# Performance work log

Hardware: AMD Instinct MI355X
Metric: run time of the kernel (lower is better)

## Reference

```python
import jax, jax.numpy as jnp
import numpy as np

NP_, NS_ = 100000, 10000      # num pdrugs / seffect nodes
FPD, FSE = 512, 768           # raw feature dims
H = 64                        # hidden_channels
E = 1_600_000                 # message-passing edges
L = 1_000_000                 # labeled edges (pos+neg)


def setup_inputs() -> dict:
    key = jax.random.key(0)
    ks = jax.random.split(key, 40)
    f32 = jnp.float32

    def nrm(k, shape, scale=0.05):
        return jax.random.normal(k, shape, f32) * scale

    inp = {}
    inp['x_pdrugs'] = jax.random.normal(ks[0], (NP_, FPD), f32)
    inp['x_seffect'] = jax.random.normal(ks[1], (NS_, FSE), f32)
    inp['node_id_pd'] = jnp.arange(NP_)
    inp['node_id_se'] = jnp.arange(NS_)
    inp['edge_index'] = jnp.stack([
        jax.random.randint(ks[2], (E,), 0, NP_),
        jax.random.randint(ks[3], (E,), 0, NS_)])
    # positive labeled edges + negative-sampled edges (label 0)
    inp['edge_label_index'] = jnp.stack([
        jax.random.randint(ks[4], (L,), 0, NP_),
        jax.random.randint(ks[5], (L,), 0, NS_)])
    inp['edge_label'] = jnp.concatenate(
        [jnp.ones(L // 2, f32), jnp.zeros(L - L // 2, f32)])

    # input projections + node embeddings
    inp['W_pd'] = nrm(ks[6], (FPD, H)); inp['b_pd'] = jnp.zeros((H,), f32)
    inp['W_se'] = nrm(ks[7], (FSE, H)); inp['b_se'] = jnp.zeros((H,), f32)
    inp['emb_pd'] = nrm(ks[8], (NP_, H), 1.0)
    inp['emb_se'] = nrm(ks[9], (NS_, H), 1.0)

    # hetero SAGEConv params: 2 layers x 2 edge types (p2s, s2p)
    i = 10
    for lyr in (1, 2):
        for et in ('p2s', 's2p'):
            inp[f'c{lyr}_{et}_Wl'] = nrm(ks[i], (H, H)); i += 1
            inp[f'c{lyr}_{et}_bl'] = jnp.zeros((H,), f32)
            inp[f'c{lyr}_{et}_Wr'] = nrm(ks[i], (H, H)); i += 1
    return inp


def _sage(x_src, x_dst, src_idx, dst_idx, n_dst, Wl, bl, Wr):
    # SAGEConv: lin_l(mean_j x_src[j]) + lin_r(x_dst)
    msg = x_src[src_idx]                                   # [E, H] gather
    agg = jax.ops.segment_sum(msg, dst_idx, num_segments=n_dst)
    deg = jax.ops.segment_sum(jnp.ones((src_idx.shape[0],), x_src.dtype),
                              dst_idx, num_segments=n_dst)
    mean = agg / jnp.clip(deg, 1.0)[:, None]
    return mean @ Wl + bl + x_dst @ Wr


def reference(x_pdrugs, x_seffect, edge_label,
              W_pd, b_pd, W_se, b_se, emb_pd, emb_se,
              c1_p2s_Wl, c1_p2s_bl, c1_p2s_Wr,
              c1_s2p_Wl, c1_s2p_bl, c1_s2p_Wr,
              c2_p2s_Wl, c2_p2s_bl, c2_p2s_Wr,
              c2_s2p_Wl, c2_s2p_bl, c2_s2p_Wr,
              node_id_pd, node_id_se, edge_index, edge_label_index):
    src, dst = edge_index[0], edge_index[1]  # pdrugs -> seffect

    # embed + linear fusion
    h_pd = x_pdrugs @ W_pd + b_pd + emb_pd[node_id_pd]
    h_se = x_seffect @ W_se + b_se + emb_se[node_id_se]

    # hetero GNN layer 1 (relu)
    se1 = jax.nn.relu(_sage(h_pd, h_se, src, dst, NS_, c1_p2s_Wl, c1_p2s_bl, c1_p2s_Wr))
    pd1 = jax.nn.relu(_sage(h_se, h_pd, dst, src, NP_, c1_s2p_Wl, c1_s2p_bl, c1_s2p_Wr))

    # hetero GNN layer 2 (no activation)
    se2 = _sage(pd1, se1, src, dst, NS_, c2_p2s_Wl, c2_p2s_bl, c2_p2s_Wr)
    pd2 = _sage(se1, pd1, dst, src, NP_, c2_s2p_Wl, c2_s2p_bl, c2_s2p_Wr)

    # edge-wise gather-dot classifier
    pred = jnp.sum(pd2[edge_label_index[0]] * se2[edge_label_index[1]], axis=-1)
    return (pred, edge_label)
```

## Files before the change

### kernel.cpp

```cpp
#include <hip/hip_runtime.h>

namespace {

constexpr int NP = 100000;
constexpr int NS = 10000;
constexpr int EC = 1600000;
constexpr int LC = 1000000;

constexpr int SH_S = 6;
constexpr int SH_P = 9;
constexpr int NBS = (NS + 63) >> SH_S;
constexpr int NBP = (NP + 511) >> SH_P;
constexpr int CHUNK = 8192;
constexpr int NBLK = (EC + CHUNK - 1) / CHUNK;

typedef short i16x8 __attribute__((ext_vector_type(8)));
typedef float f32x4 __attribute__((ext_vector_type(4)));

__device__ inline ushort f2bf(float f) {
  unsigned u = __float_as_uint(f);
  u += 0x7FFFu + ((u >> 16) & 1u);
  return (ushort)(u >> 16);
}
__device__ inline float bflo(uint v) { return __uint_as_float(v << 16); }
__device__ inline float bfhi(uint v) { return __uint_as_float(v & 0xffff0000u); }


__global__ void __launch_bounds__(256) k_bcount(const int* __restrict__ src,
                                                const int* __restrict__ dst,
                                                int* __restrict__ bcntS,
                                                int* __restrict__ bcntP, int E) {
  __shared__ int hS[256];
  __shared__ int hP[256];
  const int t = threadIdx.x;
  hS[t] = 0;
  hP[t] = 0;
  __syncthreads();
  const int base = blockIdx.x * CHUNK;
  const int end = min(base + CHUNK, E);
  for (int e = base + t; e < end; e += 256) {
    atomicAdd(&hS[dst[e] >> SH_S], 1);
    atomicAdd(&hP[src[e] >> SH_P], 1);
  }
  __syncthreads();
  if (t < NBS && hS[t]) atomicAdd(&bcntS[t], hS[t]);
  if (t < NBP && hP[t]) atomicAdd(&bcntP[t], hP[t]);
}

__global__ void __launch_bounds__(256) k_bscan(const int* __restrict__ bcntS,
                                               const int* __restrict__ bcntP,
                                               int* __restrict__ gbaseS,
                                               int* __restrict__ gbaseP,
                                               int* __restrict__ gcurS,
                                               int* __restrict__ gcurP) {
  __shared__ int s[256];
  const int t = threadIdx.x;
  int v = (t < NBS) ? bcntS[t] : 0;
  s[t] = v;
  __syncthreads();
  for (int off = 1; off < 256; off <<= 1) {
    int u = (t >= off) ? s[t - off] : 0;
    __syncthreads();
    s[t] += u;
    __syncthreads();
  }
  if (t < NBS) {
    int ex = s[t] - v;
    gbaseS[t] = ex;
    gcurS[t] = ex;
  }
  __syncthreads();
  v = (t < NBP) ? bcntP[t] : 0;
  s[t] = v;
  __syncthreads();
  for (int off = 1; off < 256; off <<= 1) {
    int u = (t >= off) ? s[t - off] : 0;
    __syncthreads();
    s[t] += u;
    __syncthreads();
  }
  if (t < NBP) {
    int ex = s[t] - v;
    gbaseP[t] = ex;
    gcurP[t] = ex;
  }
}

__global__ void __launch_bounds__(256) k_bscatter(const int* __restrict__ src,
                                                  const int* __restrict__ dst,
                                                  int* __restrict__ gcurS,
                                                  int* __restrict__ gcurP,
                                                  int* __restrict__ tmpS,
                                                  int* __restrict__ tmpP, int E) {
  __shared__ int hS[256];
  __shared__ int hP[256];
  const int t = threadIdx.x;
  hS[t] = 0;
  hP[t] = 0;
  __syncthreads();
  const int base = blockIdx.x * CHUNK;
  const int end = min(base + CHUNK, E);
  for (int e = base + t; e < end; e += 256) {
    atomicAdd(&hS[dst[e] >> SH_S], 1);
    atomicAdd(&hP[src[e] >> SH_P], 1);
  }
  __syncthreads();
  int myBaseS = 0, myBaseP = 0;
  if (t < NBS) {
    int c = hS[t];
    myBaseS = c ? atomicAdd(&gcurS[t], c) : 0;
  }
  if (t < NBP) {
    int c = hP[t];
    myBaseP = c ? atomicAdd(&gcurP[t], c) : 0;
  }
  __syncthreads();
  if (t < NBS) hS[t] = myBaseS;
  if (t < NBP) hP[t] = myBaseP;
  __syncthreads();
  for (int e = base + t; e < end; e += 256) {
    const int d = dst[e];
    const int s = src[e];
    int p = atomicAdd(&hS[d >> SH_S], 1);
    tmpS[p] = ((d & 63) << 17) | s;
    int q = atomicAdd(&hP[s >> SH_P], 1);
    tmpP[q] = ((s & 511) << 14) | d;
  }
}

template <int NN, int LBITS>
__global__ void __launch_bounds__(256) k_bfinal(const int* __restrict__ tmp,
                                                const int* __restrict__ gbase,
                                                const int* __restrict__ bcnt,
                                                int shift, int Nnodes,
                                                int* __restrict__ rowptr,
                                                int* __restrict__ deg,
                                                int* __restrict__ col) {
  __shared__ int ldeg[NN];
  __shared__ int lscan[512];
  const int b = blockIdx.x;
  const int t = threadIdx.x;
  const int n0 = b << shift;
  const int base = gbase[b];
  const int cnt = bcnt[b];
  for (int i = t; i < NN; i += 256) ldeg[i] = 0;
  __syncthreads();
  for (int j = t; j < cnt; j += 256) atomicAdd(&ldeg[tmp[base + j] >> LBITS], 1);
  __syncthreads();
  for (int i = t; i < 512; i += 256) lscan[i] = (i < NN) ? ldeg[i] : 0;
  __syncthreads();
  for (int off = 1; off < 512; off <<= 1) {
    const int i0 = t, i1 = t + 256;
    const int v0 = (i0 >= off) ? lscan[i0 - off] : 0;
    const int v1 = (i1 >= off) ? lscan[i1 - off] : 0;
    __syncthreads();
    lscan[i0] += v0;
    lscan[i1] += v1;
    __syncthreads();
  }
  for (int i = t; i < NN; i += 256) {
    const int n = n0 + i;
    if (n < Nnodes) {
      const int dg = ldeg[i];
      rowptr[n] = base + lscan[i] - dg;
      deg[n] = dg;
    }
  }
  __syncthreads();
  for (int i = t; i < NN; i += 256) lscan[i] -= ldeg[i];
  __syncthreads();
  for (int j = t; j < cnt; j += 256) {
    const int v = tmp[base + j];
    const int p = atomicAdd(&lscan[v >> LBITS], 1);
    col[base + p] = v & ((1 << LBITS) - 1);
  }
}


struct WtJob {
  const float* src;
  ushort* dst;
  int K;
  int stride;
  int off;
};
struct WtJobs {
  WtJob j[10];
};

__global__ void __launch_bounds__(256) k_wt_all(WtJobs jobs) {
  int e = blockIdx.x * 256 + threadIdx.x;
#pragma unroll
  for (int i = 0; i < 10; i++) {
    const int K = jobs.j[i].K;
    const int sz = K * 64;
    if (e < sz) {
      const int n = e / K;
      const int k = e - n * K;
      jobs.j[i].dst[(size_t)n * jobs.j[i].stride + jobs.j[i].off + k] =
          f2bf(jobs.j[i].src[(size_t)k * 64 + n]);
      return;
    }
    e -= sz;
  }
}


struct GJob {
  const void* A0;
  const void* A1;
  int KA0, sA0, sA1, K;
  const ushort* Wt;
  const float* bias;
  const float* emb;
  const int* nid;
  void* out;
  int M;
  int nblk;
};

template <bool RELU, bool EMB, bool ABF16, bool OBF16>
__global__ void __launch_bounds__(256) k_mgemm2(GJob ja, GJob jb) {
  __shared__ ushort Xs[64 * 72];
  __shared__ ushort Ws[64 * 72];
  const bool sec = (int)blockIdx.x >= ja.nblk;
  const GJob j = sec ? jb : ja;
  const int bid = sec ? ((int)blockIdx.x - ja.nblk) : (int)blockIdx.x;
  const int t = threadIdx.x;
  const int row0 = bid * 64;
  const int lane = t & 63;
  const int w = t >> 6;
  const int m16 = lane & 15;
  const int q = lane >> 4;
  const int M = j.M;
  const int K = j.K;
  const int KA0 = j.KA0;

  f32x4 acc[4];
#pragma unroll
  for (int nt = 0; nt < 4; nt++) acc[nt] = {0.f, 0.f, 0.f, 0.f};

  const int ksteps = K >> 6;
  for (int ks = 0; ks < ksteps; ks++) {
    const int k0 = ks << 6;
    uint4 wv[2];
#pragma unroll
    for (int i = 0; i < 2; i++) {
      const int u = t + i * 256;
      const int n = u >> 3;
      const int kk8 = (u & 7) << 3;
      wv[i] = *reinterpret_cast<const uint4*>(j.Wt + (size_t)n * K + k0 + kk8);
    }
    if constexpr (ABF16) {
      uint4 xv[2];
#pragma unroll
      for (int i = 0; i < 2; i++) {
        const int u = t + i * 256;
        const int row = u >> 3;
        const int k8 = (u & 7) << 3;
        const int gr = min(row0 + row, M - 1);
        const int kk = k0 + k8;
        const ushort* sp = (kk < KA0)
                               ? ((const ushort*)j.A0 + (size_t)gr * j.sA0 + kk)
                               : ((const ushort*)j.A1 + (size_t)gr * j.sA1 + (kk - KA0));
        xv[i] = *reinterpret_cast<const uint4*>(sp);
      }
      __syncthreads();
#pragma unroll
      for (int i = 0; i < 2; i++) {
        const int u = t + i * 256;
        const int row = u >> 3;
        const int k8 = (u & 7) << 3;
        *reinterpret_cast<uint4*>(&Xs[row * 72 + k8]) = xv[i];
      }
    } else {
      float4 xv[4];
#pragma unroll
      for (int i = 0; i < 4; i++) {
        const int u = t + i * 256;
        const int row = u >> 4;
        const int k4 = (u & 15) << 2;
        const int gr = min(row0 + row, M - 1);
        const int kk = k0 + k4;
        const float* sp = (kk < KA0)
                              ? ((const float*)j.A0 + (size_t)gr * j.sA0 + kk)
                              : ((const float*)j.A1 + (size_t)gr * j.sA1 + (kk - KA0));
        xv[i] = *reinterpret_cast<const float4*>(sp);
      }
      __syncthreads();
#pragma unroll
      for (int i = 0; i < 4; i++) {
        const int u = t + i * 256;
        const int row = u >> 4;
        const int k4 = (u & 15) << 2;
        ushort4 o;
        o.x = f2bf(xv[i].x);
        o.y = f2bf(xv[i].y);
        o.z = f2bf(xv[i].z);
        o.w = f2bf(xv[i].w);
        *reinterpret_cast<ushort4*>(&Xs[row * 72 + k4]) = o;
      }
    }
#pragma unroll
    for (int i = 0; i < 2; i++) {
      const int u = t + i * 256;
      const int n = u >> 3;
      const int kk8 = (u & 7) << 3;
      *reinterpret_cast<uint4*>(&Ws[n * 72 + kk8]) = wv[i];
    }
    __syncthreads();

    const ushort* ap = &Xs[(w * 16 + m16) * 72 + q * 8];
    const i16x8 a0 = *reinterpret_cast<const i16x8*>(ap);
    const i16x8 a1 = *reinterpret_cast<const i16x8*>(ap + 32);
#pragma unroll
    for (int nt = 0; nt < 4; nt++) {
      const ushort* bp = &Ws[(nt * 16 + m16) * 72 + q * 8];
      const i16x8 b0 = *reinterpret_cast<const i16x8*>(bp);
      const i16x8 b1 = *reinterpret_cast<const i16x8*>(bp + 32);
      acc[nt] = __builtin_amdgcn_mfma_f32_16x16x32_bf16(a0, b0, acc[nt], 0, 0, 0);
      acc[nt] = __builtin_amdgcn_mfma_f32_16x16x32_bf16(a1, b1, acc[nt], 0, 0, 0);
    }
    __syncthreads();
  }

  int grow[4];
  int nrow[4];
#pragma unroll
  for (int r = 0; r < 4; r++) {
    grow[r] = row0 + w * 16 + q * 4 + r;
    nrow[r] = (EMB && grow[r] < M) ? j.nid[grow[r]] : 0;
  }
#pragma unroll
  for (int nt = 0; nt < 4; nt++) {
    const int colv = nt * 16 + m16;
    const float bv = j.bias[colv];
#pragma unroll
    for (int r = 0; r < 4; r++) {
      if (grow[r] < M) {
        float v = acc[nt][r] + bv;
        if (EMB) v += j.emb[(size_t)nrow[r] * 64 + colv];
        if (RELU) v = fmaxf(v, 0.f);
        if (OBF16)
          ((ushort*)j.out)[(size_t)grow[r] * 64 + colv] = f2bf(v);
        else
          ((float*)j.out)[(size_t)grow[r] * 64 + colv] = v;
      }
    }
  }
}


__global__ void __launch_bounds__(256) k_agg2(
    const ushort* __restrict__ hS,
    const ushort* __restrict__ hP,
    const int* __restrict__ rpS, const int* __restrict__ degS, const int* __restrict__ colS,
    const int* __restrict__ rpP, const int* __restrict__ degP, const int* __restrict__ colP,
    ushort* __restrict__ outS,
    ushort* __restrict__ outP
) {
  int g = blockIdx.x * 4 + (threadIdx.x >> 6);
  const uint* hu;
  const int* rp;
  const int* deg;
  const int* col;
  uint* out;
  int node;
  if (g < NS) {
    hu = (const uint*)hS; rp = rpS; deg = degS; col = colS; out = (uint*)outS;
    node = g;
  } else {
    node = g - NS;
    if (node >= NP) return;
    hu = (const uint*)hP; rp = rpP; deg = degP; col = colP; out = (uint*)outP;
  }
  const int lane = threadIdx.x & 63;
  const int c = lane & 31;
  const int half = lane >> 5;
  const int beg = rp[node];
  const int cnt = deg[node];
  float a0 = 0.f, a1 = 0.f;
  int jj = 0;
  for (; jj + 16 <= cnt; jj += 16) {
    int n[8];
#pragma unroll
    for (int u = 0; u < 8; u++) n[u] = col[beg + jj + 2 * u + half];
#pragma unroll
    for (int u = 0; u < 8; u++) {
      const uint v = hu[(size_t)n[u] * 32 + c];
      a0 += bflo(v);
      a1 += bfhi(v);
    }
  }
  for (; jj + 2 <= cnt; jj += 2) {
    const uint v = hu[(size_t)col[beg + jj + half] * 32 + c];
    a0 += bflo(v);
    a1 += bfhi(v);
  }
  if (jj < cnt && half == 0) {
    const uint v = hu[(size_t)col[beg + jj] * 32 + c];
    a0 += bflo(v);
    a1 += bfhi(v);
  }
  a0 += __shfl_xor(a0, 32);
  a1 += __shfl_xor(a1, 32);
  if (half == 0) {
    const float d = (cnt > 0) ? (float)cnt : 1.f;
    const uint o = (uint)f2bf(a0 / d) | ((uint)f2bf(a1 / d) << 16);
    out[(size_t)node * 32 + c] = o;
  }
}


__global__ void __launch_bounds__(256) k_classify(const float* __restrict__ pd2,
                                                  const float* __restrict__ se2,
                                                  const int* __restrict__ i0,
                                                  const int* __restrict__ i1,
                                                  const float* __restrict__ elabel,
                                                  float* __restrict__ outF, int L,
                                                  int nClsBlk) {
  if ((int)blockIdx.x >= nClsBlk) {
    const int i = ((int)blockIdx.x - nClsBlk) * 256 + threadIdx.x;
    if (i < L / 4)
      reinterpret_cast<float4*>(outF + L)[i] =
          reinterpret_cast<const float4*>(elabel)[i];
    return;
  }
  const int e = blockIdx.x * 16 + (threadIdx.x >> 4);
  if (e >= L) return;
  const int l16 = threadIdx.x & 15;
  const int a = i0[e];
  const int b = i1[e];
  const float4 va = *reinterpret_cast<const float4*>(&pd2[(size_t)a * 64 + l16 * 4]);
  const float4 vb = *reinterpret_cast<const float4*>(&se2[(size_t)b * 64 + l16 * 4]);
  float v = va.x * vb.x + va.y * vb.y + va.z * vb.z + va.w * vb.w;
  v += __shfl_xor(v, 1, 16);
  v += __shfl_xor(v, 2, 16);
  v += __shfl_xor(v, 4, 16);
  v += __shfl_xor(v, 8, 16);
  if (l16 == 0) outF[e] = v;
}

}

extern "C" void kernel_launch(void* const* d_in, const int* in_sizes, int n_in,
                              void* d_out, int out_size, void* d_ws, size_t ws_size,
                              hipStream_t stream) {
  (void)in_sizes; (void)n_in; (void)out_size; (void)ws_size;
  const float* x_pd = (const float*)d_in[0];
  const float* x_se = (const float*)d_in[1];
  const int* nid_pd = (const int*)d_in[2];
  const int* nid_se = (const int*)d_in[3];
  const int* eidx = (const int*)d_in[4];
  const int* elidx = (const int*)d_in[5];
  const float* elabel = (const float*)d_in[6];
  const float* W_pd = (const float*)d_in[7];
  const float* b_pd = (const float*)d_in[8];
  const float* W_se = (const float*)d_in[9];
  const float* b_se = (const float*)d_in[10];
  const float* emb_pd = (const float*)d_in[11];
  const float* emb_se = (const float*)d_in[12];
  const float* c1_p2s_Wl = (const float*)d_in[13];
  const float* c1_p2s_bl = (const float*)d_in[14];
  const float* c1_p2s_Wr = (const float*)d_in[15];
  const float* c1_s2p_Wl = (const float*)d_in[16];
  const float* c1_s2p_bl = (const float*)d_in[17];
  const float* c1_s2p_Wr = (const float*)d_in[18];
  const float* c2_p2s_Wl = (const float*)d_in[19];
  const float* c2_p2s_bl = (const float*)d_in[20];
  const float* c2_p2s_Wr = (const float*)d_in[21];
  const float* c2_s2p_Wl = (const float*)d_in[22];
  const float* c2_s2p_bl = (const float*)d_in[23];
  const float* c2_s2p_Wr = (const float*)d_in[24];

  const int* src = eidx;
  const int* dst = eidx + EC;
  const int* li0 = elidx;
  const int* li1 = elidx + LC;

  char* ws = (char*)d_ws;
  size_t o = 0;
  auto alloc = [&](size_t bytes) -> char* {
    char* p = ws + o;
    o = (o + bytes + 255) & ~(size_t)255;
    return p;
  };
  ushort* h_pd = (ushort*)alloc((size_t)NP * 64 * 2);
  ushort* h_se = (ushort*)alloc((size_t)NS * 64 * 2);
  ushort* pd1 = (ushort*)alloc((size_t)NP * 64 * 2);
  ushort* se1 = (ushort*)alloc((size_t)NS * 64 * 2);
  ushort* agg_pd = (ushort*)alloc((size_t)NP * 64 * 2);
  ushort* agg_se = (ushort*)alloc((size_t)NS * 64 * 2);
  float* pd2 = (float*)alloc((size_t)NP * 64 * 4);
  float* se2 = (float*)alloc((size_t)NS * 64 * 4);
  int* col_se = (int*)alloc((size_t)EC * 4);
  int* col_pd = (int*)alloc((size_t)EC * 4);
  int* deg_se = (int*)alloc((size_t)NS * 4);
  int* deg_pd = (int*)alloc((size_t)NP * 4);
  int* rp_se = (int*)alloc((size_t)NS * 4);
  int* rp_pd = (int*)alloc((size_t)NP * 4);
  int* bcntS = (int*)alloc(1024);
  int* bcntP = (int*)alloc(1024);
  int* gbaseS = (int*)alloc(1024);
  int* gbaseP = (int*)alloc(1024);
  int* gcurS = (int*)alloc(1024);
  int* gcurP = (int*)alloc(1024);
  ushort* wt_pd = (ushort*)alloc((size_t)64 * 512 * 2);
  ushort* wt_se = (ushort*)alloc((size_t)64 * 768 * 2);
  ushort* wt_c1p2s = (ushort*)alloc((size_t)64 * 128 * 2);
  ushort* wt_c1s2p = (ushort*)alloc((size_t)64 * 128 * 2);
  ushort* wt_c2p2s = (ushort*)alloc((size_t)64 * 128 * 2);
  ushort* wt_c2s2p = (ushort*)alloc((size_t)64 * 128 * 2);

  int* tmpS = (int*)pd2;
  int* tmpP = tmpS + EC;

  hipMemsetAsync(bcntS, 0, 1024, stream);
  hipMemsetAsync(bcntP, 0, 1024, stream);

  k_bcount<<<NBLK, 256, 0, stream>>>(src, dst, bcntS, bcntP, EC);
  k_bscan<<<1, 256, 0, stream>>>(bcntS, bcntP, gbaseS, gbaseP, gcurS, gcurP);
  k_bscatter<<<NBLK, 256, 0, stream>>>(src, dst, gcurS, gcurP, tmpS, tmpP, EC);
  k_bfinal<64, 17><<<NBS, 256, 0, stream>>>(tmpS, gbaseS, bcntS, SH_S, NS, rp_se,
                                            deg_se, col_se);
  k_bfinal<512, 14><<<NBP, 256, 0, stream>>>(tmpP, gbaseP, bcntP, SH_P, NP, rp_pd,
                                             deg_pd, col_pd);

  {
    WtJobs jobs;
    jobs.j[0] = {W_pd, wt_pd, 512, 512, 0};
    jobs.j[1] = {W_se, wt_se, 768, 768, 0};
    jobs.j[2] = {c1_p2s_Wl, wt_c1p2s, 64, 128, 0};
    jobs.j[3] = {c1_p2s_Wr, wt_c1p2s, 64, 128, 64};
    jobs.j[4] = {c1_s2p_Wl, wt_c1s2p, 64, 128, 0};
    jobs.j[5] = {c1_s2p_Wr, wt_c1s2p, 64, 128, 64};
    jobs.j[6] = {c2_p2s_Wl, wt_c2p2s, 64, 128, 0};
    jobs.j[7] = {c2_p2s_Wr, wt_c2p2s, 64, 128, 64};
    jobs.j[8] = {c2_s2p_Wl, wt_c2s2p, 64, 128, 0};
    jobs.j[9] = {c2_s2p_Wr, wt_c2s2p, 64, 128, 64};
    const int tot = 64 * (512 + 768 + 8 * 64);
    k_wt_all<<<(tot + 255) / 256, 256, 0, stream>>>(jobs);
  }

  const int gP = (NP + 63) / 64;
  const int gS = (NS + 63) / 64;
  const int gAgg = (NS + NP) / 4;

  {
    GJob jp = {x_pd, nullptr, 512, 512, 0, 512, wt_pd, b_pd, emb_pd, nid_pd, h_pd, NP, gP};
    GJob js = {x_se, nullptr, 768, 768, 0, 768, wt_se, b_se, emb_se, nid_se, h_se, NS, gS};
    k_mgemm2<false, true, false, true><<<gP + gS, 256, 0, stream>>>(jp, js);
  }

  k_agg2<<<gAgg, 256, 0, stream>>>(h_pd, h_se, rp_se, deg_se, col_se, rp_pd, deg_pd,
                                   col_pd, agg_se, agg_pd);
  {
    GJob jp = {agg_pd, h_pd, 64, 64, 64, 128, wt_c1s2p, c1_s2p_bl, nullptr, nullptr, pd1, NP, gP};
    GJob js = {agg_se, h_se, 64, 64, 64, 128, wt_c1p2s, c1_p2s_bl, nullptr, nullptr, se1, NS, gS};
    k_mgemm2<true, false, true, true><<<gP + gS, 256, 0, stream>>>(jp, js);
  }

  k_agg2<<<gAgg, 256, 0, stream>>>(pd1, se1, rp_se, deg_se, col_se, rp_pd, deg_pd,
                                   col_pd, agg_se, agg_pd);
  {
    GJob jp = {agg_pd, pd1, 64, 64, 64, 128, wt_c2s2p, c2_s2p_bl, nullptr, nullptr, pd2, NP, gP};
    GJob js = {agg_se, se1, 64, 64, 64, 128, wt_c2p2s, c2_p2s_bl, nullptr, nullptr, se2, NS, gS};
    k_mgemm2<false, false, true, false><<<gP + gS, 256, 0, stream>>>(jp, js);
  }

  float* outF = (float*)d_out;
  const int nClsBlk = (LC + 15) / 16;
  const int nCpyBlk = (LC / 4 + 255) / 256;
  k_classify<<<nClsBlk + nCpyBlk, 256, 0, stream>>>(pd2, se2, li0, li1, elabel, outF,
                                                    LC, nClsBlk);
}
```

Before: 762.6 us.

## Bucket-sort classifier edges by drug row and load GEMM operands straight from global memory

```diff
diff --git a/kernel.cpp b/kernel.cpp
--- a/kernel.cpp
+++ b/kernel.cpp
@@ -13,6 +13,7 @@
 constexpr int NBP = (NP + 511) >> SH_P;
 constexpr int CHUNK = 8192;
 constexpr int NBLK = (EC + CHUNK - 1) / CHUNK;
+constexpr int LBLK = (LC + CHUNK - 1) / CHUNK;
 
 typedef short i16x8 __attribute__((ext_vector_type(8)));
 typedef float f32x4 __attribute__((ext_vector_type(4)));
@@ -25,14 +26,39 @@
 __device__ inline float bflo(uint v) { return __uint_as_float(v << 16); }
 __device__ inline float bfhi(uint v) { return __uint_as_float(v & 0xffff0000u); }
 
+__device__ inline i16x8 pack8(float4 a, float4 b) {
+  i16x8 r;
+  r[0] = (short)f2bf(a.x);
+  r[1] = (short)f2bf(a.y);
+  r[2] = (short)f2bf(a.z);
+  r[3] = (short)f2bf(a.w);
+  r[4] = (short)f2bf(b.x);
+  r[5] = (short)f2bf(b.y);
+  r[6] = (short)f2bf(b.z);
+  r[7] = (short)f2bf(b.w);
+  return r;
+}
+
 
 __global__ void __launch_bounds__(256) k_bcount(const int* __restrict__ src,
                                                 const int* __restrict__ dst,
+                                                const int* __restrict__ li0,
                                                 int* __restrict__ bcntS,
-                                                int* __restrict__ bcntP, int E) {
+                                                int* __restrict__ bcntP,
+                                                int* __restrict__ bcntL, int E, int L) {
   __shared__ int hS[256];
   __shared__ int hP[256];
   const int t = threadIdx.x;
+  if ((int)blockIdx.x >= NBLK) {
+    hS[t] = 0;
+    __syncthreads();
+    const int base = ((int)blockIdx.x - NBLK) * CHUNK;
+    const int end = min(base + CHUNK, L);
+    for (int e = base + t; e < end; e += 256) atomicAdd(&hS[li0[e] >> SH_P], 1);
+    __syncthreads();
+    if (t < NBP && hS[t]) atomicAdd(&bcntL[t], hS[t]);
+    return;
+  }
   hS[t] = 0;
   hP[t] = 0;
   __syncthreads();
@@ -49,10 +75,12 @@
 
 __global__ void __launch_bounds__(256) k_bscan(const int* __restrict__ bcntS,
                                                const int* __restrict__ bcntP,
+                                               const int* __restrict__ bcntL,
                                                int* __restrict__ gbaseS,
                                                int* __restrict__ gbaseP,
                                                int* __restrict__ gcurS,
-                                               int* __restrict__ gcurP) {
+                                               int* __restrict__ gcurP,
+                                               int* __restrict__ gcurL) {
   __shared__ int s[256];
   const int t = threadIdx.x;
   int v = (t < NBS) ? bcntS[t] : 0;
@@ -84,17 +112,53 @@
     gbaseP[t] = ex;
     gcurP[t] = ex;
   }
+  __syncthreads();
+  v = (t < NBP) ? bcntL[t] : 0;
+  s[t] = v;
+  __syncthreads();
+  for (int off = 1; off < 256; off <<= 1) {
+    int u = (t >= off) ? s[t - off] : 0;
+    __syncthreads();
+    s[t] += u;
+    __syncthreads();
+  }
+  if (t < NBP) gcurL[t] = s[t] - v;
 }
 
 __global__ void __launch_bounds__(256) k_bscatter(const int* __restrict__ src,
                                                   const int* __restrict__ dst,
+                                                  const int* __restrict__ li0,
                                                   int* __restrict__ gcurS,
                                                   int* __restrict__ gcurP,
+                                                  int* __restrict__ gcurL,
                                                   int* __restrict__ tmpS,
-                                                  int* __restrict__ tmpP, int E) {
+                                                  int* __restrict__ tmpP,
+                                                  int2* __restrict__ tmpL, int E, int L) {
   __shared__ int hS[256];
   __shared__ int hP[256];
   const int t = threadIdx.x;
+  if ((int)blockIdx.x >= NBLK) {
+    hS[t] = 0;
+    __syncthreads();
+    const int base = ((int)blockIdx.x - NBLK) * CHUNK;
+    const int end = min(base + CHUNK, L);
+    for (int e = base + t; e < end; e += 256) atomicAdd(&hS[li0[e] >> SH_P], 1);
+    __syncthreads();
+    int myBase = 0;
+    if (t < NBP) {
+      int c = hS[t];
+      myBase = c ? atomicAdd(&gcurL[t], c) : 0;
+    }
+    __syncthreads();
+    if (t < NBP) hS[t] = myBase;
+    __syncthreads();
+    for (int e = base + t; e < end; e += 256) {
+      const int a = li0[e];
+      int p = atomicAdd(&hS[a >> SH_P], 1);
+      tmpL[p] = make_int2(a, e);
+    }
+    return;
+  }
   hS[t] = 0;
   hP[t] = 0;
   __syncthreads();
@@ -220,14 +284,11 @@
 };
 
 template <bool RELU, bool EMB, bool ABF16, bool OBF16>
-__global__ void __launch_bounds__(256) k_mgemm2(GJob ja, GJob jb) {
-  __shared__ ushort Xs[64 * 72];
-  __shared__ ushort Ws[64 * 72];
+__global__ void __launch_bounds__(256) k_fgemm(GJob ja, GJob jb) {
   const bool sec = (int)blockIdx.x >= ja.nblk;
   const GJob j = sec ? jb : ja;
   const int bid = sec ? ((int)blockIdx.x - ja.nblk) : (int)blockIdx.x;
   const int t = threadIdx.x;
-  const int row0 = bid * 64;
   const int lane = t & 63;
   const int w = t >> 6;
   const int m16 = lane & 15;
@@ -235,100 +296,53 @@
   const int M = j.M;
   const int K = j.K;
   const int KA0 = j.KA0;
+  const int row0 = bid * 64 + w * 16;
+  const int gr = min(row0 + m16, M - 1);
 
   f32x4 acc[4];
 #pragma unroll
   for (int nt = 0; nt < 4; nt++) acc[nt] = {0.f, 0.f, 0.f, 0.f};
 
   const int ksteps = K >> 6;
+#pragma unroll 2
   for (int ks = 0; ks < ksteps; ks++) {
     const int k0 = ks << 6;
-    uint4 wv[2];
-#pragma unroll
-    for (int i = 0; i < 2; i++) {
-      const int u = t + i * 256;
-      const int n = u >> 3;
-      const int kk8 = (u & 7) << 3;
-      wv[i] = *reinterpret_cast<const uint4*>(j.Wt + (size_t)n * K + k0 + kk8);
-    }
+    i16x8 a0, a1;
     if constexpr (ABF16) {
-      uint4 xv[2];
-#pragma unroll
-      for (int i = 0; i < 2; i++) {
-        const int u = t + i * 256;
-        const int row = u >> 3;
-        const int k8 = (u & 7) << 3;
-        const int gr = min(row0 + row, M - 1);
-        const int kk = k0 + k8;
-        const ushort* sp = (kk < KA0)
-                               ? ((const ushort*)j.A0 + (size_t)gr * j.sA0 + kk)
-                               : ((const ushort*)j.A1 + (size_t)gr * j.sA1 + (kk - KA0));
-        xv[i] = *reinterpret_cast<const uint4*>(sp);
-      }
-      __syncthreads();
-#pragma unroll
-      for (int i = 0; i < 2; i++) {
-        const int u = t + i * 256;
-        const int row = u >> 3;
-        const int k8 = (u & 7) << 3;
-        *reinterpret_cast<uint4*>(&Xs[row * 72 + k8]) = xv[i];
-      }
+      const int ka = k0 + q * 8;
+      const ushort* p0 = (ka < KA0)
+                             ? ((const ushort*)j.A0 + (size_t)gr * j.sA0 + ka)
+                             : ((const ushort*)j.A1 + (size_t)gr * j.sA1 + (ka - KA0));
+      const int kb = ka + 32;
+      const ushort* p1 = (kb < KA0)
+                             ? ((const ushort*)j.A0 + (size_t)gr * j.sA0 + kb)
+                             : ((const ushort*)j.A1 + (size_t)gr * j.sA1 + (kb - KA0));
+      a0 = *reinterpret_cast<const i16x8*>(p0);
+      a1 = *reinterpret_cast<const i16x8*>(p1);
     } else {
-      float4 xv[4];
-#pragma unroll
-      for (int i = 0; i < 4; i++) {
-        const int u = t + i * 256;
-        const int row = u >> 4;
-        const int k4 = (u & 15) << 2;
-        const int gr = min(row0 + row, M - 1);
-        const int kk = k0 + k4;
-        const float* sp = (kk < KA0)
-                              ? ((const float*)j.A0 + (size_t)gr * j.sA0 + kk)
-                              : ((const float*)j.A1 + (size_t)gr * j.sA1 + (kk - KA0));
-        xv[i] = *reinterpret_cast<const float4*>(sp);
-      }
-      __syncthreads();
-#pragma unroll
-      for (int i = 0; i < 4; i++) {
-        const int u = t + i * 256;
-        const int row = u >> 4;
-        const int k4 = (u & 15) << 2;
-        ushort4 o;
-        o.x = f2bf(xv[i].x);
-        o.y = f2bf(xv[i].y);
-        o.z = f2bf(xv[i].z);
-        o.w = f2bf(xv[i].w);
-        *reinterpret_cast<ushort4*>(&Xs[row * 72 + k4]) = o;
-      }
-    }
-#pragma unroll
-    for (int i = 0; i < 2; i++) {
-      const int u = t + i * 256;
-      const int n = u >> 3;
-      const int kk8 = (u & 7) << 3;
-      *reinterpret_cast<uint4*>(&Ws[n * 72 + kk8]) = wv[i];
-    }
-    __syncthreads();
-
-    const ushort* ap = &Xs[(w * 16 + m16) * 72 + q * 8];
-    const i16x8 a0 = *reinterpret_cast<const i16x8*>(ap);
-    const i16x8 a1 = *reinterpret_cast<const i16x8*>(ap + 32);
+      const float* pa = (const float*)j.A0 + (size_t)gr * j.sA0 + k0 + q * 8;
+      const float4 f0 = *reinterpret_cast<const float4*>(pa);
+      const float4 f1 = *reinterpret_cast<const float4*>(pa + 4);
+      const float4 g0 = *reinterpret_cast<const float4*>(pa + 32);
+      const float4 g1 = *reinterpret_cast<const float4*>(pa + 36);
+      a0 = pack8(f0, f1);
+      a1 = pack8(g0, g1);
+    }
 #pragma unroll
     for (int nt = 0; nt < 4; nt++) {
-      const ushort* bp = &Ws[(nt * 16 + m16) * 72 + q * 8];
-      const i16x8 b0 = *reinterpret_cast<const i16x8*>(bp);
-      const i16x8 b1 = *reinterpret_cast<const i16x8*>(bp + 32);
+      const ushort* wb = j.Wt + (size_t)(nt * 16 + m16) * K + k0 + q * 8;
+      const i16x8 b0 = *reinterpret_cast<const i16x8*>(wb);
+      const i16x8 b1 = *reinterpret_cast<const i16x8*>(wb + 32);
       acc[nt] = __builtin_amdgcn_mfma_f32_16x16x32_bf16(a0, b0, acc[nt], 0, 0, 0);
       acc[nt] = __builtin_amdgcn_mfma_f32_16x16x32_bf16(a1, b1, acc[nt], 0, 0, 0);
     }
-    __syncthreads();
   }
 
   int grow[4];
   int nrow[4];
 #pragma unroll
   for (int r = 0; r < 4; r++) {
-    grow[r] = row0 + w * 16 + q * 4 + r;
+    grow[r] = bid * 64 + w * 16 + q * 4 + r;
     nrow[r] = (EMB && grow[r] < M) ? j.nid[grow[r]] : 0;
   }
 #pragma unroll
@@ -414,7 +428,7 @@
 
 __global__ void __launch_bounds__(256) k_classify(const float* __restrict__ pd2,
                                                   const float* __restrict__ se2,
-                                                  const int* __restrict__ i0,
+                                                  const int2* __restrict__ tmpL,
                                                   const int* __restrict__ i1,
                                                   const float* __restrict__ elabel,
                                                   float* __restrict__ outF, int L,
@@ -429,8 +443,10 @@
   const int e = blockIdx.x * 16 + (threadIdx.x >> 4);
   if (e >= L) return;
   const int l16 = threadIdx.x & 15;
-  const int a = i0[e];
-  const int b = i1[e];
+  const int2 pr = tmpL[e];
+  const int a = pr.x;
+  const int idx = pr.y;
+  const int b = i1[idx];
   const float4 va = *reinterpret_cast<const float4*>(&pd2[(size_t)a * 64 + l16 * 4]);
   const float4 vb = *reinterpret_cast<const float4*>(&se2[(size_t)b * 64 + l16 * 4]);
   float v = va.x * vb.x + va.y * vb.y + va.z * vb.z + va.w * vb.w;
@@ -438,7 +454,7 @@
   v += __shfl_xor(v, 2, 16);
   v += __shfl_xor(v, 4, 16);
   v += __shfl_xor(v, 8, 16);
-  if (l16 == 0) outF[e] = v;
+  if (l16 == 0) outF[idx] = v;
 }
 
 }
@@ -495,16 +511,19 @@
   float* se2 = (float*)alloc((size_t)NS * 64 * 4);
   int* col_se = (int*)alloc((size_t)EC * 4);
   int* col_pd = (int*)alloc((size_t)EC * 4);
+  int2* tmpL = (int2*)alloc((size_t)LC * 8);
   int* deg_se = (int*)alloc((size_t)NS * 4);
   int* deg_pd = (int*)alloc((size_t)NP * 4);
   int* rp_se = (int*)alloc((size_t)NS * 4);
   int* rp_pd = (int*)alloc((size_t)NP * 4);
   int* bcntS = (int*)alloc(1024);
   int* bcntP = (int*)alloc(1024);
+  int* bcntL = (int*)alloc(1024);
   int* gbaseS = (int*)alloc(1024);
   int* gbaseP = (int*)alloc(1024);
   int* gcurS = (int*)alloc(1024);
   int* gcurP = (int*)alloc(1024);
+  int* gcurL = (int*)alloc(1024);
   ushort* wt_pd = (ushort*)alloc((size_t)64 * 512 * 2);
   ushort* wt_se = (ushort*)alloc((size_t)64 * 768 * 2);
   ushort* wt_c1p2s = (ushort*)alloc((size_t)64 * 128 * 2);
@@ -515,12 +534,13 @@
   int* tmpS = (int*)pd2;
   int* tmpP = tmpS + EC;
 
-  hipMemsetAsync(bcntS, 0, 1024, stream);
-  hipMemsetAsync(bcntP, 0, 1024, stream);
-
-  k_bcount<<<NBLK, 256, 0, stream>>>(src, dst, bcntS, bcntP, EC);
-  k_bscan<<<1, 256, 0, stream>>>(bcntS, bcntP, gbaseS, gbaseP, gcurS, gcurP);
-  k_bscatter<<<NBLK, 256, 0, stream>>>(src, dst, gcurS, gcurP, tmpS, tmpP, EC);
+  hipMemsetAsync(bcntS, 0, 3072, stream);
+
+  k_bcount<<<NBLK + LBLK, 256, 0, stream>>>(src, dst, li0, bcntS, bcntP, bcntL, EC, LC);
+  k_bscan<<<1, 256, 0, stream>>>(bcntS, bcntP, bcntL, gbaseS, gbaseP, gcurS, gcurP,
+                                 gcurL);
+  k_bscatter<<<NBLK + LBLK, 256, 0, stream>>>(src, dst, li0, gcurS, gcurP, gcurL, tmpS,
+                                              tmpP, tmpL, EC, LC);
   k_bfinal<64, 17><<<NBS, 256, 0, stream>>>(tmpS, gbaseS, bcntS, SH_S, NS, rp_se,
                                             deg_se, col_se);
   k_bfinal<512, 14><<<NBP, 256, 0, stream>>>(tmpP, gbaseP, bcntP, SH_P, NP, rp_pd,
@@ -549,7 +569,7 @@
   {
     GJob jp = {x_pd, nullptr, 512, 512, 0, 512, wt_pd, b_pd, emb_pd, nid_pd, h_pd, NP, gP};
     GJob js = {x_se, nullptr, 768, 768, 0, 768, wt_se, b_se, emb_se, nid_se, h_se, NS, gS};
-    k_mgemm2<false, true, false, true><<<gP + gS, 256, 0, stream>>>(jp, js);
+    k_fgemm<false, true, false, true><<<gP + gS, 256, 0, stream>>>(jp, js);
   }
 
   k_agg2<<<gAgg, 256, 0, stream>>>(h_pd, h_se, rp_se, deg_se, col_se, rp_pd, deg_pd,
@@ -557,7 +577,7 @@
   {
     GJob jp = {agg_pd, h_pd, 64, 64, 64, 128, wt_c1s2p, c1_s2p_bl, nullptr, nullptr, pd1, NP, gP};
     GJob js = {agg_se, h_se, 64, 64, 64, 128, wt_c1p2s, c1_p2s_bl, nullptr, nullptr, se1, NS, gS};
-    k_mgemm2<true, false, true, true><<<gP + gS, 256, 0, stream>>>(jp, js);
+    k_fgemm<true, false, true, true><<<gP + gS, 256, 0, stream>>>(jp, js);
   }
 
   k_agg2<<<gAgg, 256, 0, stream>>>(pd1, se1, rp_se, deg_se, col_se, rp_pd, deg_pd,
@@ -565,12 +585,12 @@
   {
     GJob jp = {agg_pd, pd1, 64, 64, 64, 128, wt_c2s2p, c2_s2p_bl, nullptr, nullptr, pd2, NP, gP};
     GJob js = {agg_se, se1, 64, 64, 64, 128, wt_c2p2s, c2_p2s_bl, nullptr, nullptr, se2, NS, gS};
-    k_mgemm2<false, false, true, false><<<gP + gS, 256, 0, stream>>>(jp, js);
+    k_fgemm<false, false, true, false><<<gP + gS, 256, 0, stream>>>(jp, js);
   }
 
   float* outF = (float*)d_out;
   const int nClsBlk = (LC + 15) / 16;
   const int nCpyBlk = (LC / 4 + 255) / 256;
-  k_classify<<<nClsBlk + nCpyBlk, 256, 0, stream>>>(pd2, se2, li0, li1, elabel, outF,
+  k_classify<<<nClsBlk + nCpyBlk, 256, 0, stream>>>(pd2, se2, tmpL, li1, elabel, outF,
                                                     LC, nClsBlk);
 }
```

New measurement: 765.6 us. About the same (+0.4%).

## Bucket labeled edges by drug index for classifier locality; swizzle GEMM blocks

Applied to the files above, without the earlier changes.

```diff
diff --git a/kernel.cpp b/kernel.cpp
--- a/kernel.cpp
+++ b/kernel.cpp
@@ -13,6 +13,7 @@
 constexpr int NBP = (NP + 511) >> SH_P;
 constexpr int CHUNK = 8192;
 constexpr int NBLK = (EC + CHUNK - 1) / CHUNK;
+constexpr int LBLK = (LC + CHUNK - 1) / CHUNK;
 
 typedef short i16x8 __attribute__((ext_vector_type(8)));
 typedef float f32x4 __attribute__((ext_vector_type(4)));
@@ -28,11 +29,23 @@
 
 __global__ void __launch_bounds__(256) k_bcount(const int* __restrict__ src,
                                                 const int* __restrict__ dst,
+                                                const int* __restrict__ li0,
                                                 int* __restrict__ bcntS,
-                                                int* __restrict__ bcntP, int E) {
+                                                int* __restrict__ bcntP,
+                                                int* __restrict__ bcntL, int E, int L) {
   __shared__ int hS[256];
   __shared__ int hP[256];
   const int t = threadIdx.x;
+  if ((int)blockIdx.x >= NBLK) {
+    hS[t] = 0;
+    __syncthreads();
+    const int base = ((int)blockIdx.x - NBLK) * CHUNK;
+    const int end = min(base + CHUNK, L);
+    for (int e = base + t; e < end; e += 256) atomicAdd(&hS[li0[e] >> SH_P], 1);
+    __syncthreads();
+    if (t < NBP && hS[t]) atomicAdd(&bcntL[t], hS[t]);
+    return;
+  }
   hS[t] = 0;
   hP[t] = 0;
   __syncthreads();
@@ -49,10 +62,12 @@
 
 __global__ void __launch_bounds__(256) k_bscan(const int* __restrict__ bcntS,
                                                const int* __restrict__ bcntP,
+                                               const int* __restrict__ bcntL,
                                                int* __restrict__ gbaseS,
                                                int* __restrict__ gbaseP,
                                                int* __restrict__ gcurS,
-                                               int* __restrict__ gcurP) {
+                                               int* __restrict__ gcurP,
+                                               int* __restrict__ gcurL) {
   __shared__ int s[256];
   const int t = threadIdx.x;
   int v = (t < NBS) ? bcntS[t] : 0;
@@ -84,17 +99,53 @@
     gbaseP[t] = ex;
     gcurP[t] = ex;
   }
+  __syncthreads();
+  v = (t < NBP) ? bcntL[t] : 0;
+  s[t] = v;
+  __syncthreads();
+  for (int off = 1; off < 256; off <<= 1) {
+    int u = (t >= off) ? s[t - off] : 0;
+    __syncthreads();
+    s[t] += u;
+    __syncthreads();
+  }
+  if (t < NBP) gcurL[t] = s[t] - v;
 }
 
 __global__ void __launch_bounds__(256) k_bscatter(const int* __restrict__ src,
                                                   const int* __restrict__ dst,
+                                                  const int* __restrict__ li0,
                                                   int* __restrict__ gcurS,
                                                   int* __restrict__ gcurP,
+                                                  int* __restrict__ gcurL,
                                                   int* __restrict__ tmpS,
-                                                  int* __restrict__ tmpP, int E) {
+                                                  int* __restrict__ tmpP,
+                                                  int2* __restrict__ tmpL, int E, int L) {
   __shared__ int hS[256];
   __shared__ int hP[256];
   const int t = threadIdx.x;
+  if ((int)blockIdx.x >= NBLK) {
+    hS[t] = 0;
+    __syncthreads();
+    const int base = ((int)blockIdx.x - NBLK) * CHUNK;
+    const int end = min(base + CHUNK, L);
+    for (int e = base + t; e < end; e += 256) atomicAdd(&hS[li0[e] >> SH_P], 1);
+    __syncthreads();
+    int myBase = 0;
+    if (t < NBP) {
+      int c = hS[t];
+      myBase = c ? atomicAdd(&gcurL[t], c) : 0;
+    }
+    __syncthreads();
+    if (t < NBP) hS[t] = myBase;
+    __syncthreads();
+    for (int e = base + t; e < end; e += 256) {
+      const int a = li0[e];
+      int p = atomicAdd(&hS[a >> SH_P], 1);
+      tmpL[p] = make_int2(a, e);
+    }
+    return;
+  }
   hS[t] = 0;
   hP[t] = 0;
   __syncthreads();
@@ -223,9 +274,12 @@
 __global__ void __launch_bounds__(256) k_mgemm2(GJob ja, GJob jb) {
   __shared__ ushort Xs[64 * 72];
   __shared__ ushort Ws[64 * 72];
-  const bool sec = (int)blockIdx.x >= ja.nblk;
+  const int nwg = ja.nblk + jb.nblk;
+  int bswz = (int)blockIdx.x;
+  if ((nwg & 7) == 0) bswz = (bswz & 7) * (nwg >> 3) + (bswz >> 3);
+  const bool sec = bswz >= ja.nblk;
   const GJob j = sec ? jb : ja;
-  const int bid = sec ? ((int)blockIdx.x - ja.nblk) : (int)blockIdx.x;
+  const int bid = sec ? (bswz - ja.nblk) : bswz;
   const int t = threadIdx.x;
   const int row0 = bid * 64;
   const int lane = t & 63;
@@ -414,7 +468,7 @@
 
 __global__ void __launch_bounds__(256) k_classify(const float* __restrict__ pd2,
                                                   const float* __restrict__ se2,
-                                                  const int* __restrict__ i0,
+                                                  const int2* __restrict__ tmpL,
                                                   const int* __restrict__ i1,
                                                   const float* __restrict__ elabel,
                                                   float* __restrict__ outF, int L,
@@ -429,8 +483,10 @@
   const int e = blockIdx.x * 16 + (threadIdx.x >> 4);
   if (e >= L) return;
   const int l16 = threadIdx.x & 15;
-  const int a = i0[e];
-  const int b = i1[e];
+  const int2 pr = tmpL[e];
+  const int a = pr.x;
+  const int idx = pr.y;
+  const int b = i1[idx];
   const float4 va = *reinterpret_cast<const float4*>(&pd2[(size_t)a * 64 + l16 * 4]);
   const float4 vb = *reinterpret_cast<const float4*>(&se2[(size_t)b * 64 + l16 * 4]);
   float v = va.x * vb.x + va.y * vb.y + va.z * vb.z + va.w * vb.w;
@@ -438,7 +494,7 @@
   v += __shfl_xor(v, 2, 16);
   v += __shfl_xor(v, 4, 16);
   v += __shfl_xor(v, 8, 16);
-  if (l16 == 0) outF[e] = v;
+  if (l16 == 0) outF[idx] = v;
 }
 
 }
@@ -495,16 +551,19 @@
   float* se2 = (float*)alloc((size_t)NS * 64 * 4);
   int* col_se = (int*)alloc((size_t)EC * 4);
   int* col_pd = (int*)alloc((size_t)EC * 4);
+  int2* tmpL = (int2*)alloc((size_t)LC * 8);
   int* deg_se = (int*)alloc((size_t)NS * 4);
   int* deg_pd = (int*)alloc((size_t)NP * 4);
   int* rp_se = (int*)alloc((size_t)NS * 4);
   int* rp_pd = (int*)alloc((size_t)NP * 4);
   int* bcntS = (int*)alloc(1024);
   int* bcntP = (int*)alloc(1024);
+  int* bcntL = (int*)alloc(1024);
   int* gbaseS = (int*)alloc(1024);
   int* gbaseP = (int*)alloc(1024);
   int* gcurS = (int*)alloc(1024);
   int* gcurP = (int*)alloc(1024);
+  int* gcurL = (int*)alloc(1024);
   ushort* wt_pd = (ushort*)alloc((size_t)64 * 512 * 2);
   ushort* wt_se = (ushort*)alloc((size_t)64 * 768 * 2);
   ushort* wt_c1p2s = (ushort*)alloc((size_t)64 * 128 * 2);
@@ -515,12 +574,13 @@
   int* tmpS = (int*)pd2;
   int* tmpP = tmpS + EC;
 
-  hipMemsetAsync(bcntS, 0, 1024, stream);
-  hipMemsetAsync(bcntP, 0, 1024, stream);
-
-  k_bcount<<<NBLK, 256, 0, stream>>>(src, dst, bcntS, bcntP, EC);
-  k_bscan<<<1, 256, 0, stream>>>(bcntS, bcntP, gbaseS, gbaseP, gcurS, gcurP);
-  k_bscatter<<<NBLK, 256, 0, stream>>>(src, dst, gcurS, gcurP, tmpS, tmpP, EC);
+  hipMemsetAsync(bcntS, 0, 3072, stream);
+
+  k_bcount<<<NBLK + LBLK, 256, 0, stream>>>(src, dst, li0, bcntS, bcntP, bcntL, EC, LC);
+  k_bscan<<<1, 256, 0, stream>>>(bcntS, bcntP, bcntL, gbaseS, gbaseP, gcurS, gcurP,
+                                 gcurL);
+  k_bscatter<<<NBLK + LBLK, 256, 0, stream>>>(src, dst, li0, gcurS, gcurP, gcurL, tmpS,
+                                              tmpP, tmpL, EC, LC);
   k_bfinal<64, 17><<<NBS, 256, 0, stream>>>(tmpS, gbaseS, bcntS, SH_S, NS, rp_se,
                                             deg_se, col_se);
   k_bfinal<512, 14><<<NBP, 256, 0, stream>>>(tmpP, gbaseP, bcntP, SH_P, NP, rp_pd,
@@ -571,6 +631,6 @@
   float* outF = (float*)d_out;
   const int nClsBlk = (LC + 15) / 16;
   const int nCpyBlk = (LC / 4 + 255) / 256;
-  k_classify<<<nClsBlk + nCpyBlk, 256, 0, stream>>>(pd2, se2, li0, li1, elabel, outF,
+  k_classify<<<nClsBlk + nCpyBlk, 256, 0, stream>>>(pd2, se2, tmpL, li1, elabel, outF,
                                                     LC, nClsBlk);
 }
```

After: 787.0 us. +3.2%, slower.
